# Optimization experiments

Hardware: AMD Instinct MI355X
Metric: run time of the kernel (lower is better)

Reference implementation:

```python
import jax, jax.numpy as jnp
import numpy as np

# Model dims
P_SPECS = [(6, 256), (7, 256)]          # pattern_length -> num_patterns (ordered)
P = 512                                  # total_num_patterns
MAXL = 7                                 # max_pattern_length
ND = 2                                   # num_diags (self-loop diag + main diag)
D = 300                                  # embedding_dim
V = 50000                                # vocab size
B = 32                                   # batch size
T = 128                                  # max_doc_len
NC = 2                                   # num_classes
NEG = -1e30                              # max-sum semiring zero; one = 0.0
END_STATES = np.concatenate([np.full(n, l - 1, dtype=np.int32) for l, n in P_SPECS])


def setup_inputs() -> dict:
    key = jax.random.key(0)
    ks = jax.random.split(key, 8)
    tokens = jax.random.randint(ks[0], (B, T), 0, V, dtype=jnp.int32)
    doc_lens = jax.random.randint(ks[1], (B,), 64, T + 1, dtype=jnp.int32)
    emb_table = jax.random.normal(ks[2], (V, D), dtype=jnp.float32)
    diags = jax.random.normal(ks[3], (P * ND * MAXL, D), dtype=jnp.float32)
    diags = diags / jnp.linalg.norm(diags, axis=1, keepdims=True)  # normalize(diags)
    bias = jax.random.normal(ks[4], (P * ND * MAXL, 1), dtype=jnp.float32)
    epsilons = jax.random.normal(ks[5], (P, MAXL - 1), dtype=jnp.float32)
    bn_weight = jnp.ones((P,), jnp.float32)
    bn_bias = jnp.zeros((P,), jnp.float32)
    final_w = 0.05 * jax.random.normal(ks[6], (NC, P), dtype=jnp.float32)
    final_b = jnp.zeros((NC,), jnp.float32)
    return dict(tokens=tokens, doc_lens=doc_lens, emb_table=emb_table, diags=diags,
                bias=bias, epsilons=epsilons, bn_weight=bn_weight, bn_bias=bn_bias,
                final_w=final_w, final_b=final_b)


def reference(tokens, doc_lens, emb_table, diags, bias, epsilons,
              bn_weight, bn_bias, final_w, final_b):
    # --- transition matrices (max-sum semiring: from_outer is identity) ---
    emb = emb_table[tokens]                                   # [B,T,D]
    # mm(diags, embeddings) + bias_scale * bias  (bias_scale = 1.0)
    ts = jnp.einsum('btd,kd->btk', emb, diags) + bias[:, 0]   # [B,T,P*ND*MAXL]
    ts = ts.reshape(B, T, P, ND, MAXL)                        # [B,T,P,ND,MAXL]

    end = jnp.asarray(END_STATES)                             # [P]
    hid0 = jnp.full((B, P, MAXL), NEG, jnp.float32).at[:, :, 0].set(0.0)
    sc0 = jnp.full((B, P), NEG, jnp.float32)                  # semiring.zero
    zpad = jnp.full((B, P, 1), NEG, jnp.float32)              # zero_padding
    rpad = jnp.zeros((B, P, 1), jnp.float32)                  # restart_padding (one)

    # epsilon_values = epsilon_scale (one=0) + epsilons
    def step(carry, xs):
        hid, sc = carry
        tm, i = xs                                            # tm: [B,P,ND,MAXL]
        # epsilon transitions
        ae = jnp.maximum(hid, jnp.concatenate([zpad, hid[:, :, :-1] + epsilons], axis=2))
        # main path: diag index -1 (the main diagonal)
        main = jnp.concatenate([rpad, ae[:, :, :-1] + tm[:, :, -1, :-1]], axis=2)
        # self loops: diag 0, self_loop_scale = semiring.one = 0
        sl = ae + tm[:, :, 0, :]
        hid = jnp.maximum(main, sl)
        endv = jnp.take_along_axis(hid, jnp.broadcast_to(end[None, :, None], (B, P, 1)), axis=2)[:, :, 0]
        sc = jnp.where((doc_lens > i)[:, None], jnp.maximum(sc, endv), sc)
        return (hid, sc), None

    (_, scores), _ = jax.lax.scan(step, (hid0, sc0),
                                  (jnp.moveaxis(ts, 1, 0), jnp.arange(T, dtype=jnp.int32)))

    # BatchNorm1d (training mode: biased batch statistics)
    mean = scores.mean(axis=0)
    var = scores.var(axis=0)
    scores = (scores - mean) * jax.lax.rsqrt(var + 1e-5) * bn_weight + bn_bias
    # binarize_scores
    scores = jnp.sign(jax.nn.relu(scores))
    # final linear layer
    return scores @ final_w.T + final_b                       # [B, NC]
```

## Files before the change

### kernel.cpp

```cpp
#include <hip/hip_runtime.h>

#define BB 32
#define TT 128
#define PP 512
#define DD 300
#define KT 10
#define NR 13
#define NN 6656
#define AT 256
#define BT 416
#define NEG -1e30f

typedef _Float16 half8 __attribute__((ext_vector_type(8)));
typedef float floatx4 __attribute__((ext_vector_type(4)));

__device__ __forceinline__ void async_load16(const void* g, void* l) {
    __builtin_amdgcn_global_load_lds(
        (const __attribute__((address_space(1))) void*)g,
        (__attribute__((address_space(3))) void*)l, 16, 0, 0);
}

__device__ __forceinline__ floatx4 mfma16(half8 a, half8 b, floatx4 c) {
    return __builtin_amdgcn_mfma_f32_16x16x32_f16(a, b, c, 0, 0, 0);
}

__global__ __launch_bounds__(256) void pack_kernel(
    const int* __restrict__ tokens, const float* __restrict__ emb,
    const float* __restrict__ diags, const float* __restrict__ bias,
    _Float16* __restrict__ AhP, _Float16* __restrict__ AlP,
    _Float16* __restrict__ BhP, _Float16* __restrict__ BlP)
{
    const int idx = blockIdx.x * 256 + threadIdx.x;
    if (idx >= (AT + BT) * KT * 64) return;
    const int chunk = idx >> 6;
    const int ln = idx & 63;

    const float* src;
    float kslot;
    _Float16 *dh, *dl;
    int kt;
    if (chunk < AT * KT) {
        const int mt = chunk / KT; kt = chunk - mt * KT;
        const int m = mt * 16 + (ln & 15);
        src = emb + (size_t)tokens[m] * DD;
        kslot = 1.0f;
        dh = AhP + (size_t)chunk * 512 + ln * 8;
        dl = AlP + (size_t)chunk * 512 + ln * 8;
    } else {
        const int c2 = chunk - AT * KT;
        const int nt = c2 / KT; kt = c2 - nt * KT;
        const int n = nt * 16 + (ln & 15);
        const int p = n / NR;
        const int srow = p * 14 + (n - p * NR);
        src = diags + (size_t)srow * DD;
        kslot = bias[srow];
        dh = BhP + (size_t)c2 * 512 + ln * 8;
        dl = BlP + (size_t)c2 * 512 + ln * 8;
    }

    const int k0 = kt * 32 + (ln >> 4) * 8;
    float v[8];
    if (k0 + 8 <= DD) {
        float4 a = *(const float4*)(src + k0);
        float4 b = *(const float4*)(src + k0 + 4);
        v[0] = a.x; v[1] = a.y; v[2] = a.z; v[3] = a.w;
        v[4] = b.x; v[5] = b.y; v[6] = b.z; v[7] = b.w;
    } else {
        #pragma unroll
        for (int i = 0; i < 8; ++i) {
            const int k = k0 + i;
            v[i] = (k < DD) ? src[k] : (k == DD ? kslot : 0.f);
        }
    }
    half8 h, l;
    #pragma unroll
    for (int i = 0; i < 8; ++i) {
        h[i] = (_Float16)v[i];
        l[i] = (_Float16)((v[i] - (float)h[i]) * 4096.f);
    }
    *(half8*)dh = h;
    *(half8*)dl = l;
}

__global__ __launch_bounds__(256, 2) void gemm_kernel(
    const _Float16* __restrict__ AhP, const _Float16* __restrict__ AlP,
    const _Float16* __restrict__ BhP, const _Float16* __restrict__ BlP,
    float* __restrict__ C)
{
    __shared__ __align__(16) _Float16 Bs[2][2][8][512];

    const int tid = threadIdx.x;
    const int w = tid >> 6, ln = tid & 63;
    const int n0t = blockIdx.x * 8, m0t = blockIdx.y * 8;
    const int wm = w & 1, wn = w >> 1;

    floatx4 acc0[4][4], acc1[4][4];
    #pragma unroll
    for (int i = 0; i < 4; ++i)
        #pragma unroll
        for (int j = 0; j < 4; ++j) {
            acc0[i][j] = (floatx4){0.f, 0.f, 0.f, 0.f};
            acc1[i][j] = (floatx4){0.f, 0.f, 0.f, 0.f};
        }

    half8 ah[2][4], al[2][4];

    auto loadA = [&](int kt, int pb) {
        #pragma unroll
        for (int i = 0; i < 4; ++i) {
            const size_t ch = ((size_t)(m0t + wm * 4 + i) * KT + kt) * 512 + ln * 8;
            ah[pb][i] = *(const half8*)(AhP + ch);
            al[pb][i] = *(const half8*)(AlP + ch);
        }
    };
    auto stageB = [&](int kt, int buf) {
        #pragma unroll
        for (int s = 0; s < 2; ++s) {
            const int nt = w + s * 4;
            const size_t ch = ((size_t)(n0t + nt) * KT + kt) * 512 + ln * 8;
            async_load16(BhP + ch, &Bs[buf][0][nt][0]);
            async_load16(BlP + ch, &Bs[buf][1][nt][0]);
        }
    };

    stageB(0, 0);
    loadA(0, 0);
    __syncthreads();

    #pragma unroll
    for (int kt = 0; kt < KT; ++kt) {
        const int cb = kt & 1, nb = cb ^ 1;
        if (kt + 1 < KT) {
            loadA(kt + 1, nb);
            stageB(kt + 1, nb);
        }
        #pragma unroll
        for (int j = 0; j < 4; ++j) {
            const half8 bh = *(const half8*)&Bs[cb][0][wn * 4 + j][ln * 8];
            const half8 bl = *(const half8*)&Bs[cb][1][wn * 4 + j][ln * 8];
            #pragma unroll
            for (int i = 0; i < 4; ++i) {
                acc0[i][j] = mfma16(ah[cb][i], bh, acc0[i][j]);
                acc1[i][j] = mfma16(ah[cb][i], bl, acc1[i][j]);
                acc1[i][j] = mfma16(al[cb][i], bh, acc1[i][j]);
            }
        }
        __syncthreads();
    }

    #pragma unroll
    for (int j = 0; j < 4; ++j) {
        const int n = (n0t + wn * 4 + j) * 16 + (ln & 15);
        #pragma unroll
        for (int i = 0; i < 4; ++i) {
            const int mb = (m0t + wm * 4 + i) * 16 + (ln >> 4) * 4;
            #pragma unroll
            for (int r = 0; r < 4; ++r)
                C[(size_t)(mb + r) * NN + n] =
                    acc0[i][j][r] + acc1[i][j][r] * (1.0f / 4096.0f);
        }
    }
}

__global__ __launch_bounds__(256, 2) void scan_kernel(
    const float* __restrict__ C,
    const float* __restrict__ epsilons,
    const int* __restrict__ doc_lens,
    float* __restrict__ scores)
{
    __shared__ float smaps[64][256];

    const int tid = threadIdx.x;
    const int ln = tid & 63;
    const int ch = tid >> 6;
    const int b = blockIdx.x, pg = blockIdx.y;
    const int p = pg * 64 + ln;
    const int dl = doc_lens[b];
    const bool end5 = (p < 256);

    float e[6];
    #pragma unroll
    for (int i = 0; i < 6; ++i) e[i] = epsilons[p * 6 + i];

    float A[7][7], c[7], S[7], s0;
    #pragma unroll
    for (int i = 0; i < 7; ++i) {
        #pragma unroll
        for (int j = 0; j < 7; ++j) A[i][j] = (i == j) ? 0.f : NEG;
        c[i] = NEG; S[i] = NEG;
    }
    s0 = NEG;

    const float* base = C + (size_t)(b * 128 + ch * 32) * NN + p * NR;

    float vb[2][NR];
    {
        #pragma unroll
        for (int i = 0; i < NR; ++i) vb[0][i] = base[i];
    }

    #pragma unroll
    for (int s = 0; s < 32; ++s) {
        if (s + 1 < 32) {
            const float* src = base + (size_t)(s + 1) * NN;
            #pragma unroll
            for (int i = 0; i < NR; ++i) vb[(s + 1) & 1][i] = src[i];
        }
        const float* v = vb[s & 1];
        #pragma unroll
        for (int l = 6; l >= 1; --l) {
            const float el = e[l - 1];
            #pragma unroll
            for (int j = 0; j < 7; ++j) A[l][j] = fmaxf(A[l][j], A[l - 1][j] + el);
            c[l] = fmaxf(c[l], c[l - 1] + el);
        }
        #pragma unroll
        for (int l = 6; l >= 1; --l) {
            const float wl = v[7 + l - 1], vl = v[l];
            #pragma unroll
            for (int j = 0; j < 7; ++j)
                A[l][j] = fmaxf(A[l - 1][j] + wl, A[l][j] + vl);
            c[l] = fmaxf(c[l - 1] + wl, c[l] + vl);
        }
        #pragma unroll
        for (int j = 0; j < 7; ++j) A[0][j] += v[0];
        c[0] = fmaxf(c[0] + v[0], 0.f);
        const int t = ch * 32 + s;
        if (t < dl) {
            #pragma unroll
            for (int j = 0; j < 7; ++j)
                S[j] = fmaxf(S[j], end5 ? A[5][j] : A[6][j]);
            s0 = fmaxf(s0, end5 ? c[5] : c[6]);
        }
    }

    #pragma unroll
    for (int i = 0; i < 7; ++i) {
        #pragma unroll
        for (int j = 0; j < 7; ++j) smaps[i * 7 + j][tid] = A[i][j];
        smaps[49 + i][tid] = c[i];
        smaps[56 + i][tid] = S[i];
    }
    smaps[63][tid] = s0;
    __syncthreads();

    if (ch == 0) {
        float h[7];
        h[0] = 0.f;
        #pragma unroll
        for (int i = 1; i < 7; ++i) h[i] = NEG;
        float sc = NEG;
        #pragma unroll
        for (int cc = 0; cc < 4; ++cc) {
            const int src = cc * 64 + ln;
            float m = smaps[63][src];
            #pragma unroll
            for (int j = 0; j < 7; ++j) m = fmaxf(m, smaps[56 + j][src] + h[j]);
            sc = fmaxf(sc, m);
            float nh[7];
            #pragma unroll
            for (int i = 0; i < 7; ++i) {
                float x = smaps[49 + i][src];
                #pragma unroll
                for (int j = 0; j < 7; ++j)
                    x = fmaxf(x, smaps[i * 7 + j][src] + h[j]);
                nh[i] = x;
            }
            #pragma unroll
            for (int i = 0; i < 7; ++i) h[i] = nh[i];
        }
        scores[p * BB + b] = sc;
    }
}

__global__ __launch_bounds__(512) void finalize_kernel(
    const float* __restrict__ scores,
    const float* __restrict__ bn_w,
    const float* __restrict__ bn_b,
    const float* __restrict__ fw,
    const float* __restrict__ fb,
    float* __restrict__ out)
{
    __shared__ float acc[64];
    const int p = threadIdx.x;
    if (p < 64) acc[p] = 0.f;
    __syncthreads();

    float x[32];
    const float4* sp = (const float4*)(scores + p * 32);
    #pragma unroll
    for (int i = 0; i < 8; ++i) ((float4*)x)[i] = sp[i];

    float mean = 0.f;
    #pragma unroll
    for (int i = 0; i < 32; ++i) mean += x[i];
    mean *= (1.f / 32.f);
    float var = 0.f;
    #pragma unroll
    for (int i = 0; i < 32; ++i) { const float d = x[i] - mean; var = fmaf(d, d, var); }
    var *= (1.f / 32.f);

    const float scale = (1.f / sqrtf(var + 1e-5f)) * bn_w[p];
    const float shift = bn_b[p];
    const float w0 = fw[p], w1 = fw[PP + p];

    for (int b = 0; b < 32; ++b) {
        const float v = (x[b] - mean) * scale + shift;
        const bool bin = v > 0.f;
        float v0 = bin ? w0 : 0.f;
        float v1 = bin ? w1 : 0.f;
        #pragma unroll
        for (int o = 32; o; o >>= 1) {
            v0 += __shfl_xor(v0, o);
            v1 += __shfl_xor(v1, o);
        }
        if ((threadIdx.x & 63) == 0) {
            atomicAdd(&acc[b * 2 + 0], v0);
            atomicAdd(&acc[b * 2 + 1], v1);
        }
    }
    __syncthreads();
    if (p < 64) out[p] = acc[p] + fb[p & 1];
}

extern "C" void kernel_launch(void* const* d_in, const int* in_sizes, int n_in,
                              void* d_out, int out_size, void* d_ws, size_t ws_size,
                              hipStream_t stream) {
    const int*   tokens   = (const int*)d_in[0];
    const int*   doc_lens = (const int*)d_in[1];
    const float* emb      = (const float*)d_in[2];
    const float* diags    = (const float*)d_in[3];
    const float* bias     = (const float*)d_in[4];
    const float* eps      = (const float*)d_in[5];
    const float* bnw      = (const float*)d_in[6];
    const float* bnb      = (const float*)d_in[7];
    const float* fw       = (const float*)d_in[8];
    const float* fb       = (const float*)d_in[9];
    float* out = (float*)d_out;

    float* ts     = (float*)d_ws;
    float* scores = ts + (size_t)4096 * NN;
    _Float16* AhP = (_Float16*)(scores + PP * BB);
    _Float16* AlP = AhP + (size_t)AT * KT * 512;
    _Float16* BhP = AlP + (size_t)AT * KT * 512;
    _Float16* BlP = BhP + (size_t)BT * KT * 512;

    pack_kernel<<<(AT + BT) * KT * 64 / 256, 256, 0, stream>>>(
        tokens, emb, diags, bias, AhP, AlP, BhP, BlP);
    gemm_kernel<<<dim3(BT / 8, AT / 8), 256, 0, stream>>>(AhP, AlP, BhP, BlP, ts);
    scan_kernel<<<dim3(BB, PP / 64), 256, 0, stream>>>(ts, eps, doc_lens, scores);
    finalize_kernel<<<1, 512, 0, stream>>>(scores, bnw, bnb, fw, fb, out);
}
```

Before: 204.3 us.

## Merge split-fp16 GEMM accumulators, stage A-low in LDS, swizzle block order

The residual scale drops from 4096 to 64, so the hi*lo cross terms can be pre-scaled by 1/64 in fp16 and summed into a single accumulator set. This halves accumulator registers and lets launch bounds rise to 3 blocks per SM. The A-low operand now goes through LDS via async loads instead of registers, and a 1D grid with a swizzled block-to-tile mapping aims to improve L2 reuse. The risks are lost precision from the smaller residual scale, fp16 rounding of the pre-scaled operands, and extra LDS traffic.

```diff
diff --git a/kernel.cpp b/kernel.cpp
--- a/kernel.cpp
+++ b/kernel.cpp
@@ -76,73 +76,84 @@
     #pragma unroll
     for (int i = 0; i < 8; ++i) {
         h[i] = (_Float16)v[i];
-        l[i] = (_Float16)((v[i] - (float)h[i]) * 4096.f);
+        l[i] = (_Float16)((v[i] - (float)h[i]) * 64.f);
     }
     *(half8*)dh = h;
     *(half8*)dl = l;
 }
 
-__global__ __launch_bounds__(256, 2) void gemm_kernel(
+__global__ __launch_bounds__(256, 3) void gemm_kernel(
     const _Float16* __restrict__ AhP, const _Float16* __restrict__ AlP,
     const _Float16* __restrict__ BhP, const _Float16* __restrict__ BlP,
     float* __restrict__ C)
 {
-    __shared__ __align__(16) _Float16 Bs[2][2][8][512];
+    __shared__ __align__(16) _Float16 AsL[2][8 * 512];
+    __shared__ __align__(16) _Float16 BsH[2][8 * 512];
+    __shared__ __align__(16) _Float16 BsL[2][8 * 512];
 
     const int tid = threadIdx.x;
     const int w = tid >> 6, ln = tid & 63;
-    const int n0t = blockIdx.x * 8, m0t = blockIdx.y * 8;
+    const int bid = blockIdx.x;
+    const int m0t = ((bid & 7) * 4 + ((bid >> 3) & 3)) * 8;
+    const int n0t = (bid >> 5) * 8;
     const int wm = w & 1, wn = w >> 1;
 
-    floatx4 acc0[4][4], acc1[4][4];
+    floatx4 acc[4][4];
     #pragma unroll
     for (int i = 0; i < 4; ++i)
         #pragma unroll
-        for (int j = 0; j < 4; ++j) {
-            acc0[i][j] = (floatx4){0.f, 0.f, 0.f, 0.f};
-            acc1[i][j] = (floatx4){0.f, 0.f, 0.f, 0.f};
-        }
-
-    half8 ah[2][4], al[2][4];
-
-    auto loadA = [&](int kt, int pb) {
+        for (int j = 0; j < 4; ++j) acc[i][j] = (floatx4){0.f, 0.f, 0.f, 0.f};
+
+    half8 ah[2][4];
+
+    auto loadAh = [&](int kt, int pb) {
         #pragma unroll
         for (int i = 0; i < 4; ++i) {
             const size_t ch = ((size_t)(m0t + wm * 4 + i) * KT + kt) * 512 + ln * 8;
             ah[pb][i] = *(const half8*)(AhP + ch);
-            al[pb][i] = *(const half8*)(AlP + ch);
         }
     };
-    auto stageB = [&](int kt, int buf) {
+    auto stage = [&](int kt, int buf) {
         #pragma unroll
         for (int s = 0; s < 2; ++s) {
             const int nt = w + s * 4;
-            const size_t ch = ((size_t)(n0t + nt) * KT + kt) * 512 + ln * 8;
-            async_load16(BhP + ch, &Bs[buf][0][nt][0]);
-            async_load16(BlP + ch, &Bs[buf][1][nt][0]);
+            const size_t cb_ = ((size_t)(n0t + nt) * KT + kt) * 512 + ln * 8;
+            const size_t ca_ = ((size_t)(m0t + nt) * KT + kt) * 512 + ln * 8;
+            async_load16(BhP + cb_, &BsH[buf][nt * 512]);
+            async_load16(BlP + cb_, &BsL[buf][nt * 512]);
+            async_load16(AlP + ca_, &AsL[buf][nt * 512]);
         }
     };
 
-    stageB(0, 0);
-    loadA(0, 0);
+    stage(0, 0);
+    loadAh(0, 0);
     __syncthreads();
+
+    const _Float16 s6 = (_Float16)0.015625f;
 
     #pragma unroll
     for (int kt = 0; kt < KT; ++kt) {
         const int cb = kt & 1, nb = cb ^ 1;
         if (kt + 1 < KT) {
-            loadA(kt + 1, nb);
-            stageB(kt + 1, nb);
+            loadAh(kt + 1, nb);
+            stage(kt + 1, nb);
+        }
+        half8 alr[4], ahs[4];
+        #pragma unroll
+        for (int i = 0; i < 4; ++i) {
+            alr[i] = *(const half8*)&AsL[cb][(wm * 4 + i) * 512 + ln * 8];
+            ahs[i] = ah[cb][i] * s6;
         }
         #pragma unroll
         for (int j = 0; j < 4; ++j) {
-            const half8 bh = *(const half8*)&Bs[cb][0][wn * 4 + j][ln * 8];
-            const half8 bl = *(const half8*)&Bs[cb][1][wn * 4 + j][ln * 8];
+            const half8 bh = *(const half8*)&BsH[cb][(wn * 4 + j) * 512 + ln * 8];
+            const half8 bl = *(const half8*)&BsL[cb][(wn * 4 + j) * 512 + ln * 8];
+            const half8 bhs = bh * s6;
             #pragma unroll
             for (int i = 0; i < 4; ++i) {
-                acc0[i][j] = mfma16(ah[cb][i], bh, acc0[i][j]);
-                acc1[i][j] = mfma16(ah[cb][i], bl, acc1[i][j]);
-                acc1[i][j] = mfma16(al[cb][i], bh, acc1[i][j]);
+                acc[i][j] = mfma16(ah[cb][i], bh, acc[i][j]);
+                acc[i][j] = mfma16(alr[i], bhs, acc[i][j]);
+                acc[i][j] = mfma16(ahs[i], bl, acc[i][j]);
             }
         }
         __syncthreads();
@@ -156,8 +167,7 @@
             const int mb = (m0t + wm * 4 + i) * 16 + (ln >> 4) * 4;
             #pragma unroll
             for (int r = 0; r < 4; ++r)
-                C[(size_t)(mb + r) * NN + n] =
-                    acc0[i][j][r] + acc1[i][j][r] * (1.0f / 4096.0f);
+                C[(size_t)(mb + r) * NN + n] = acc[i][j][r];
         }
     }
 }
@@ -347,7 +357,7 @@
 
     pack_kernel<<<(AT + BT) * KT * 64 / 256, 256, 0, stream>>>(
         tokens, emb, diags, bias, AhP, AlP, BhP, BlP);
-    gemm_kernel<<<dim3(BT / 8, AT / 8), 256, 0, stream>>>(AhP, AlP, BhP, BlP, ts);
+    gemm_kernel<<<dim3(BT / 8 * AT / 8), 256, 0, stream>>>(AhP, AlP, BhP, BlP, ts);
     scan_kernel<<<dim3(BB, PP / 64), 256, 0, stream>>>(ts, eps, doc_lens, scores);
     finalize_kernel<<<1, 512, 0, stream>>>(scores, bnw, bnb, fw, fb, out);
 }
```

Measured after the change: 211.9 us. +3.7%, slower.
